# Performance work log

Hardware: AMD Instinct MI355X
Metric: run time of the kernel (lower is better)

## Reference

```python
import jax, jax.numpy as jnp
import numpy as np

EPS = 1e-7
BLOCK = 64  # block_size from init_kwargs


def project(x):
    norm = jnp.clip(jnp.linalg.norm(x, axis=-1, keepdims=True), EPS)
    return jnp.where(norm >= 1.0, x / norm * (1.0 - EPS), x)


def mobius_add(x, y, c):
    x2 = jnp.sum(x * x, -1, keepdims=True)
    y2 = jnp.sum(y * y, -1, keepdims=True)
    xy = jnp.sum(x * y, -1, keepdims=True)
    num = (1 + 2 * c * xy + c * y2) * x + (1 - c * x2) * y
    den = 1 + 2 * c * xy + c * c * x2 * y2
    return project(num / jnp.clip(den, EPS))


def logmap0(y, c):
    sqrt_c = jnp.clip(jnp.sqrt(c), EPS)
    yn = jnp.linalg.norm(y, axis=-1, keepdims=True)
    mag = jnp.arctanh(jnp.minimum(yn, 1.0 - EPS)) / sqrt_c
    return jnp.where(yn < EPS, jnp.zeros_like(y), mag * (y / jnp.clip(yn, EPS)))


def expmap0(v, c):
    sqrt_c = jnp.clip(jnp.sqrt(c), EPS)
    vn = jnp.linalg.norm(v, axis=-1, keepdims=True)
    mag = jnp.tanh(sqrt_c * jnp.clip(vn, EPS)) / sqrt_c
    return project(jnp.where(vn < EPS, jnp.zeros_like(v), mag * (v / jnp.clip(vn, EPS))))


def pdist(x, y, c):
    # x: [B,H,S,1,D], y: [B,H,1,S,D], c: [1,H,1,1,1] -> [B,H,S,S]
    sqrt_c = jnp.clip(jnp.sqrt(c), EPS)
    add_norm = jnp.linalg.norm(mobius_add(-x, y, c), axis=-1)
    sc = jnp.squeeze(sqrt_c, -1)
    arg = jnp.minimum(sc * add_norm, 1.0 - EPS)
    return 2.0 * jnp.arctanh(arg) / sc


def layernorm(x, scale, bias, eps=1e-6):
    mu = jnp.mean(x, -1, keepdims=True)
    var = jnp.mean(jnp.square(x - mu), -1, keepdims=True)
    return (x - mu) * jax.lax.rsqrt(var + eps) * scale + bias


def precompute_freqs_cis(dim, end, theta=10000.0):
    f = 1.0 / theta ** (jnp.arange(0, dim, 2, dtype=jnp.float32) / dim)
    return jnp.exp(1j * jnp.outer(jnp.arange(end), f))


def rope(x, fc):
    # split-half rotary, as in WubuBlock.apply_rotary_emb
    xr, xi = jnp.split(x, 2, -1)
    xc = jax.lax.complex(xr, xi) * fc.reshape(1, 1, fc.shape[0], fc.shape[1])
    return jnp.concatenate([xc.real, xc.imag], -1)


def setup_inputs() -> dict:
    key = jax.random.key(0)
    ks = jax.random.split(key, 8)
    B, N, D, H = 1, 1024, 512, 8
    w = lambda k, shape, s=0.02: jax.random.normal(k, shape, jnp.float32) * s
    return {
        'x': w(ks[0], (B, N, D), 0.02),  # points well inside the Poincare ball
        'c_global': jax.random.uniform(ks[1], (B, 1), jnp.float32, 0.5, 1.5),
        'W_qkv': w(ks[2], (D, 3 * D)), 'b_qkv': jnp.zeros((3 * D,), jnp.float32),
        'W_out': w(ks[3], (D, D)), 'b_out': jnp.zeros((D,), jnp.float32),
        'ln1_scale': jnp.ones((D,), jnp.float32), 'ln1_bias': jnp.zeros((D,), jnp.float32),
        'ln2_scale': jnp.ones((D,), jnp.float32), 'ln2_bias': jnp.zeros((D,), jnp.float32),
        'W_ff1': w(ks[4], (D, 4 * D)), 'b_ff1': jnp.zeros((4 * D,), jnp.float32),
        'W_ff2': w(ks[5], (4 * D, D)), 'b_ff2': jnp.zeros((D,), jnp.float32),
        'c_per_head_logits': jnp.zeros((H,), jnp.float32),
        'geo_scale': jnp.ones((1, H, 1, 1), jnp.float32),
        'start_pos': 0,
    }


def reference(x, c_global, W_qkv, b_qkv, W_out, b_out, ln1_scale, ln1_bias,
              ln2_scale, ln2_bias, W_ff1, b_ff1, W_ff2, b_ff2,
              c_per_head_logits, geo_scale, start_pos):
    B, N, D = x.shape
    H = c_per_head_logits.shape[0]
    hd = D // H
    S = BLOCK
    nb = N // S
    Be = B * nb
    xb = x.reshape(Be, S, D)
    c_b = jnp.repeat(c_global, nb, axis=0).reshape(Be, 1, 1)

    # tangent-space layernorm (norm1) then logmap to tangent for QKV proj
    xn = expmap0(layernorm(logmap0(xb, c_b), ln1_scale, ln1_bias), c_b)
    xt = logmap0(xn, c_b)
    qkv = (xt @ W_qkv + b_qkv).reshape(Be, S, 3, H, hd).transpose(2, 0, 3, 1, 4)
    q, k, v = qkv[0], qkv[1], qkv[2]  # [Be,H,S,hd]

    fc = precompute_freqs_cis(hd, S)
    q = rope(q, fc)
    k = rope(k, fc)

    c_h = jax.nn.softplus(c_per_head_logits).reshape(1, H, 1, 1)
    qh = expmap0(q, c_h)
    kh = expmap0(k, c_h)

    # full pairwise hyperbolic distance: [Be,H,S,S]
    d = pdist(qh[:, :, :, None, :], kh[:, :, None, :, :], c_h[:, :, None, :, :])
    attn = jax.nn.softmax(-geo_scale * d, axis=-1)
    ao = jnp.einsum('bhqk,bhkd->bhqd', attn, v)
    ao = ao.transpose(0, 2, 1, 3).reshape(Be, S, D)

    ah = expmap0(ao @ W_out + b_out, c_b)
    xa = mobius_add(xb, ah, c_b)  # hyperbolic residual

    # hyperbolic FFN with tangent-space norm (norm2)
    xn2 = expmap0(layernorm(logmap0(xa, c_b), ln2_scale, ln2_bias), c_b)
    t = logmap0(xn2, c_b)
    fh = expmap0(jax.nn.gelu(t @ W_ff1 + b_ff1) @ W_ff2 + b_ff2, c_b)
    out = mobius_add(xa, fh, c_b)
    return out.reshape(B, N, D)
```

## Files before the change

kernel.cpp:

```cpp
#include <hip/hip_runtime.h>
#include <math.h>

#define DEV __device__ __forceinline__
typedef _Float16 h16;
typedef __attribute__((ext_vector_type(8))) _Float16 h8v;
typedef __attribute__((ext_vector_type(4))) _Float16 h4v;
typedef __attribute__((ext_vector_type(4))) float f4v;

constexpr int NTOK = 1024;
constexpr int D    = 512;
constexpr int H    = 8;
constexpr int NB   = 16;
constexpr double EPSd = 1e-7;

DEV double wave_sum(double v) {
#pragma unroll
  for (int m = 32; m; m >>= 1) v += __shfl_xor(v, m, 64);
  return v;
}

__global__ void k_prep(const float* __restrict__ Wqkv, const float* __restrict__ Wout,
                       const float* __restrict__ Wff1, const float* __restrict__ Wff2,
                       const float* __restrict__ x, const float* __restrict__ cg,
                       const float* __restrict__ s1, const float* __restrict__ b1,
                       h16* __restrict__ qT, h16* __restrict__ oT,
                       h16* __restrict__ f1T, h16* __restrict__ f2T,
                       h16* __restrict__ xt) {
  __shared__ float t[32][33];
  const int bid = blockIdx.x;
  if (bid < 3072) {
    const float* src; h16* dh; int K, N, bx, by;
    if (bid < 768)       { src = Wqkv; dh = qT;  K = 512;  N = 1536; bx = bid % 48;          by = bid / 48; }
    else if (bid < 1024) { src = Wout; dh = oT;  K = 512;  N = 512;  bx = (bid - 768) % 16;  by = (bid - 768) / 16; }
    else if (bid < 2048) { src = Wff1; dh = f1T; K = 512;  N = 2048; bx = (bid - 1024) % 64; by = (bid - 1024) / 64; }
    else                 { src = Wff2; dh = f2T; K = 2048; N = 512;  bx = (bid - 2048) % 16; by = (bid - 2048) / 16; }
    const int n0 = bx * 32, k0 = by * 32;
    const int tx = threadIdx.x & 31, ty = threadIdx.x >> 5;
    for (int i = ty; i < 32; i += 8) t[i][tx] = src[(size_t)(k0 + i) * N + n0 + tx];
    __syncthreads();
    for (int i = ty; i < 32; i += 8)
      dh[(size_t)(n0 + i) * K + k0 + tx] = (h16)t[tx][i];
    return;
  }
  const int wid = threadIdx.x >> 6, lane = threadIdx.x & 63;
  const int tok = (bid - 3072) * 4 + wid;
  const float4* xr = (const float4*)(x + (size_t)tok * D);
  float4 xv0 = xr[lane], xv1 = xr[lane + 64];
  double sv = 0.0, svv = 0.0;
  {
    const float e[8] = {xv0.x, xv0.y, xv0.z, xv0.w, xv1.x, xv1.y, xv1.z, xv1.w};
#pragma unroll
    for (int j = 0; j < 8; ++j) { double d = e[j]; sv += d; svv += d * d; }
  }
  sv = wave_sum(sv); svv = wave_sum(svv);
  double c = (double)cg[0];
  double sc = sqrt(c); if (sc < EPSd) sc = EPSd;
  double yn = sqrt(svv);
  double arg0 = yn; if (arg0 > 1.0 - EPSd) arg0 = 1.0 - EPSd;
  double f = (yn < EPSd) ? 0.0 : atanh(arg0) / sc / fmax(yn, EPSd);
  double mu = f * sv / D;
  double var = f * f * svv / D - mu * mu;
  double rs = 1.0 / sqrt(var + 1e-6);
  const float4* s1r = (const float4*)s1;
  const float4* b1r = (const float4*)b1;
  float4 sA = s1r[lane], sB = s1r[lane + 64];
  float4 bA = b1r[lane], bB = b1r[lane + 64];
  double w[8]; double sww = 0.0;
  {
    const float e[8]  = {xv0.x, xv0.y, xv0.z, xv0.w, xv1.x, xv1.y, xv1.z, xv1.w};
    const float se[8] = {sA.x, sA.y, sA.z, sA.w, sB.x, sB.y, sB.z, sB.w};
    const float be[8] = {bA.x, bA.y, bA.z, bA.w, bB.x, bB.y, bB.z, bB.w};
#pragma unroll
    for (int j = 0; j < 8; ++j) {
      w[j] = (f * (double)e[j] - mu) * rs * (double)se[j] + (double)be[j];
      sww += w[j] * w[j];
    }
  }
  sww = wave_sum(sww);
  double vn = sqrt(sww);
  double F = 0.0;
  if (vn >= EPSd) {
    double mag_e = tanh(sc * fmax(vn, EPSd)) / sc;
    F = atanh(fmin(mag_e, 1.0 - EPSd)) / (sc * vn);
  }
  h16* dst = xt + (size_t)tok * D;
#pragma unroll
  for (int half = 0; half < 2; ++half) {
    h4v o;
#pragma unroll
    for (int e = 0; e < 4; ++e) o[e] = (h16)(float)(F * w[half * 4 + e]);
    *(h4v*)(dst + 4 * (lane + 64 * half)) = o;
  }
}

DEV void stage_tile(const h16* __restrict__ gbase, int rowstride, h16* lds,
                    int wid, int lane) {
#pragma unroll
  for (int j = 0; j < 2; ++j) {
    const int rbase = wid * 16 + j * 8;
    const int grow = rbase + (lane >> 3);
    const int gch = (lane & 7) ^ (lane >> 3);
    const h16* gp = gbase + (size_t)grow * rowstride + gch * 8;
    __builtin_amdgcn_global_load_lds(
        (const __attribute__((address_space(1))) void*)gp,
        (__attribute__((address_space(3))) void*)(lds + rbase * 64), 16, 0, 0);
  }
}
DEV h8v read_frag(const h16* lds, int row, int c) {
  const int p = c ^ (row & 7);
  return *(const h8v*)(lds + row * 64 + p * 8);
}

template <int GELU, int OHALF, int SPLITK>
__global__ __launch_bounds__(256) void k_mm(
    const h16* __restrict__ A, const h16* __restrict__ B,
    const float* __restrict__ bias, float* __restrict__ Cf, h16* __restrict__ Ch,
    int M, int N, int K) {
  __shared__ __align__(16) h16 As[2][64 * 64];
  __shared__ __align__(16) h16 Bs[2][64 * 64];
  const int tid = threadIdx.x;
  const int lane = tid & 63, wid = tid >> 6;
  const int wr = (wid >> 1) * 32, wc = (wid & 1) * 32;
  const int lr = lane & 15, lg = lane >> 4;
  const size_t r0 = (size_t)blockIdx.y * 64, c0 = (size_t)blockIdx.x * 64;
  const int kz = SPLITK ? blockIdx.z : 0;
  const int Keff = SPLITK ? (K >> 1) : K;
  const f4v z = {0.f, 0.f, 0.f, 0.f};
  f4v acc[2][2]; acc[0][0] = z; acc[0][1] = z; acc[1][0] = z; acc[1][1] = z;
  const h16* Abase = A + r0 * K + (size_t)kz * Keff;
  const h16* Bbase = B + c0 * K + (size_t)kz * Keff;
  const int NT = Keff >> 6;
  stage_tile(Abase, K, As[0], wid, lane);
  stage_tile(Bbase, K, Bs[0], wid, lane);
  __syncthreads();
  int cur = 0;
  for (int t = 0; t < NT; ++t) {
    const int nxt = cur ^ 1;
    if (t + 1 < NT) {
      stage_tile(Abase + (t + 1) * 64, K, As[nxt], wid, lane);
      stage_tile(Bbase + (t + 1) * 64, K, Bs[nxt], wid, lane);
    }
    const h16* Ac = As[cur];
    const h16* Bc = Bs[cur];
#pragma unroll
    for (int ks = 0; ks < 2; ++ks) {
      const int c = ks * 4 + lg;
      h8v a0 = read_frag(Ac, wr + lr, c);
      h8v a1 = read_frag(Ac, wr + 16 + lr, c);
      h8v b0 = read_frag(Bc, wc + lr, c);
      h8v b1 = read_frag(Bc, wc + 16 + lr, c);
      acc[0][0] = __builtin_amdgcn_mfma_f32_16x16x32_f16(a0, b0, acc[0][0], 0, 0, 0);
      acc[0][1] = __builtin_amdgcn_mfma_f32_16x16x32_f16(a0, b1, acc[0][1], 0, 0, 0);
      acc[1][0] = __builtin_amdgcn_mfma_f32_16x16x32_f16(a1, b0, acc[1][0], 0, 0, 0);
      acc[1][1] = __builtin_amdgcn_mfma_f32_16x16x32_f16(a1, b1, acc[1][1], 0, 0, 0);
    }
    __syncthreads();
    cur = nxt;
  }
  float* Cfo = Cf + (size_t)kz * M * N;
#pragma unroll
  for (int m = 0; m < 2; ++m)
#pragma unroll
    for (int n = 0; n < 2; ++n) {
      const size_t row = r0 + wr + m * 16 + lg * 4;
      const size_t col = c0 + wc + n * 16 + lr;
      const float bv = (SPLITK && kz) ? 0.f : bias[col];
#pragma unroll
      for (int e = 0; e < 4; ++e) {
        float v = acc[m][n][e] + bv;
        if (GELU) {
          float x3 = v * v * v;
          v = 0.5f * v * (1.0f + tanhf(0.7978845608028654f * (v + 0.044715f * x3)));
        }
        if (OHALF) Ch[(row + e) * N + col] = (h16)v;
        else       Cfo[(row + e) * N + col] = v;
      }
    }
}

__global__ __launch_bounds__(256) void k_attn(
    const h16* __restrict__ qkv, const float* __restrict__ chl,
    const float* __restrict__ geo, h16* __restrict__ ao) {
  __shared__ __align__(16) float Qs[64][68];
  __shared__ __align__(16) float Kt[64][68];
  __shared__ __align__(16) float Vs[64][68];
  __shared__ float q2s[64], k2s[64], fqv[64], fkv[64];
  const int be = blockIdx.x >> 3, h = blockIdx.x & 7;
  const int tid = threadIdx.x;
  const double chd = log1p(exp((double)chl[h]));
  const float ch = (float)chd;
  float sc = (float)sqrt(chd); if (sc < 1e-7f) sc = 1e-7f;
  for (int l = tid; l < 64 * 32; l += 256) {
    int s = l >> 5, j = l & 31;
    const h16* base = qkv + (size_t)(be * 64 + s) * 1536 + h * 64;
    float qa = (float)base[j],       qb = (float)base[j + 32];
    float ka = (float)base[512 + j], kb = (float)base[512 + j + 32];
    float fj = expf((float)j * -0.2878231366242557f);
    float th = (float)s * fj;
    float st, ct; sincosf(th, &st, &ct);
    Qs[s][j]      = qa * ct - qb * st;
    Qs[s][j + 32] = qa * st + qb * ct;
    Kt[j][s]      = ka * ct - kb * st;
    Kt[j + 32][s] = ka * st + kb * ct;
    Vs[s][j]      = (float)base[1024 + j];
    Vs[s][j + 32] = (float)base[1024 + j + 32];
  }
  __syncthreads();
  if (tid < 128) {
    int i = tid & 63;
    float a = 0.f;
    if (tid < 64) { for (int d2 = 0; d2 < 64; ++d2) { float v = Qs[i][d2]; a += v * v; } }
    else          { for (int d2 = 0; d2 < 64; ++d2) { float v = Kt[d2][i]; a += v * v; } }
    float n = sqrtf(a);
    float m = tanhf(sc * fmaxf(n, 1e-7f)) / sc;
    float f = (n < 1e-7f) ? 0.f : m / fmaxf(n, 1e-7f);
    if (m >= 1.f) f *= (1.f - 1e-7f) / m;
    float fn = f * n;
    if (tid < 64) { fqv[i] = f; q2s[i] = fn * fn; }
    else          { fkv[i] = f; k2s[i] = fn * fn; }
  }
  __syncthreads();
  const int i = tid >> 2, g = tid & 3;
  float gacc[16];
#pragma unroll
  for (int jj = 0; jj < 16; ++jj) gacc[jj] = 0.f;
  for (int d2 = 0; d2 < 64; ++d2) {
    float qv = Qs[i][d2];
    const float4* kp = (const float4*)&Kt[d2][g * 16];
    float4 k0 = kp[0], k1 = kp[1], k2 = kp[2], k3 = kp[3];
    gacc[0] += qv * k0.x; gacc[1] += qv * k0.y; gacc[2] += qv * k0.z; gacc[3] += qv * k0.w;
    gacc[4] += qv * k1.x; gacc[5] += qv * k1.y; gacc[6] += qv * k1.z; gacc[7] += qv * k1.w;
    gacc[8] += qv * k2.x; gacc[9] += qv * k2.y; gacc[10] += qv * k2.z; gacc[11] += qv * k2.w;
    gacc[12] += qv * k3.x; gacc[13] += qv * k3.y; gacc[14] += qv * k3.z; gacc[15] += qv * k3.w;
  }
  const float gs = geo[h];
  const float q2 = q2s[i], fqi = fqv[i];
  float lg[16];
  float mx = -1e30f;
#pragma unroll
  for (int jj = 0; jj < 16; ++jj) {
    float gq = fqi * fkv[g * 16 + jj] * gacc[jj];
    float k2 = k2s[g * 16 + jj];
    float A  = 1.f - 2.f * ch * gq + ch * k2;
    float Bv = 1.f - ch * q2;
    float n2 = fmaxf(A * A * q2 - 2.f * A * Bv * gq + Bv * Bv * k2, 0.f);
    float den = fmaxf(1.f - 2.f * ch * gq + ch * ch * q2 * k2, 1e-7f);
    float r = fminf(sqrtf(n2) / den, 1.f - 1e-7f);
    float arg = fminf(sc * r, 1.f - 1e-7f);
    float l = -gs * (2.f * atanhf(arg) / sc);
    lg[jj] = l; mx = fmaxf(mx, l);
  }
  mx = fmaxf(mx, __shfl_xor(mx, 1, 64));
  mx = fmaxf(mx, __shfl_xor(mx, 2, 64));
  float pv[16]; float sum = 0.f;
#pragma unroll
  for (int jj = 0; jj < 16; ++jj) { pv[jj] = expf(lg[jj] - mx); sum += pv[jj]; }
  sum += __shfl_xor(sum, 1, 64);
  sum += __shfl_xor(sum, 2, 64);
  float inv = 1.0f / sum;
  __syncthreads();
#pragma unroll
  for (int jj = 0; jj < 16; ++jj) Qs[i][g * 16 + jj] = pv[jj] * inv;
  __syncthreads();
  float oacc[16];
#pragma unroll
  for (int dd = 0; dd < 16; ++dd) oacc[dd] = 0.f;
  for (int jv = 0; jv < 64; ++jv) {
    float p = Qs[i][jv];
    const float4* vp = (const float4*)&Vs[jv][g * 16];
    float4 v0 = vp[0], v1 = vp[1], v2 = vp[2], v3 = vp[3];
    oacc[0] += p * v0.x; oacc[1] += p * v0.y; oacc[2] += p * v0.z; oacc[3] += p * v0.w;
    oacc[4] += p * v1.x; oacc[5] += p * v1.y; oacc[6] += p * v1.z; oacc[7] += p * v1.w;
    oacc[8] += p * v2.x; oacc[9] += p * v2.y; oacc[10] += p * v2.z; oacc[11] += p * v2.w;
    oacc[12] += p * v3.x; oacc[13] += p * v3.y; oacc[14] += p * v3.z; oacc[15] += p * v3.w;
  }
#pragma unroll
  for (int dd = 0; dd < 16; ++dd)
    ao[(size_t)(be * 64 + i) * D + h * 64 + g * 16 + dd] = (h16)oacc[dd];
}

__global__ void k_resid(const float* __restrict__ x, const float* __restrict__ proj,
                        const float* __restrict__ cg, const float* __restrict__ s2,
                        const float* __restrict__ b2, float* __restrict__ xa,
                        h16* __restrict__ t2) {
  const int wid = threadIdx.x >> 6, lane = threadIdx.x & 63;
  const int tok = blockIdx.x * 4 + wid;
  const float4* xr  = (const float4*)(x + (size_t)tok * D);
  const float4* p0r = (const float4*)(proj + (size_t)tok * D);
  const float4* p1r = (const float4*)(proj + (size_t)NTOK * D + (size_t)tok * D);
  float4 xv0 = xr[lane], xv1 = xr[lane + 64];
  float4 pa0 = p0r[lane], pa1 = p0r[lane + 64];
  float4 pb0 = p1r[lane], pb1 = p1r[lane + 64];
  float pe[8], xe[8];
  xe[0]=xv0.x; xe[1]=xv0.y; xe[2]=xv0.z; xe[3]=xv0.w; xe[4]=xv1.x; xe[5]=xv1.y; xe[6]=xv1.z; xe[7]=xv1.w;
  pe[0]=pa0.x+pb0.x; pe[1]=pa0.y+pb0.y; pe[2]=pa0.z+pb0.z; pe[3]=pa0.w+pb0.w;
  pe[4]=pa1.x+pb1.x; pe[5]=pa1.y+pb1.y; pe[6]=pa1.z+pb1.z; pe[7]=pa1.w+pb1.w;
  double sx = 0, sp = 0, xx = 0, pp = 0, xp = 0;
#pragma unroll
  for (int j = 0; j < 8; ++j) {
    double dx = xe[j], dp = pe[j];
    sx += dx; sp += dp; xx += dx * dx; pp += dp * dp; xp += dx * dp;
  }
  sx = wave_sum(sx); sp = wave_sum(sp); xx = wave_sum(xx);
  pp = wave_sum(pp); xp = wave_sum(xp);
  double c = (double)cg[0];
  double sc = sqrt(c); if (sc < EPSd) sc = EPSd;
  double pn = sqrt(pp);
  double me = tanh(sc * fmax(pn, EPSd)) / sc;
  double fs = (pn < EPSd) ? 0.0 : me / fmax(pn, EPSd);
  if (me >= 1.0) fs *= (1.0 - EPSd) / me;
  double y2 = fs * fs * pp, xy = fs * xp;
  double a = 1.0 + 2.0 * c * xy + c * y2;
  double b = 1.0 - c * xx;
  double den = 1.0 + 2.0 * c * xy + c * c * xx * y2;
  if (den < EPSd) den = EPSd;
  double zn = sqrt(fmax(a * a * xx + 2.0 * a * b * xy + b * b * y2, 0.0)) / den;
  double zs = 1.0 / den;
  if (zn >= 1.0) zs *= (1.0 - EPSd) / zn;
  double xan = (zn >= 1.0) ? (1.0 - EPSd) : zn;
  double A0 = zs * a, B0 = zs * b * fs;
  double xav[8];
#pragma unroll
  for (int j = 0; j < 8; ++j) xav[j] = A0 * (double)xe[j] + B0 * (double)pe[j];
  {
    float4 o0 = {(float)xav[0], (float)xav[1], (float)xav[2], (float)xav[3]};
    float4 o1 = {(float)xav[4], (float)xav[5], (float)xav[6], (float)xav[7]};
    float4* xw = (float4*)(xa + (size_t)tok * D);
    xw[lane] = o0; xw[lane + 64] = o1;
  }
  double sxa  = A0 * sx + B0 * sp;
  double sxa2 = A0 * A0 * xx + 2.0 * A0 * B0 * xp + B0 * B0 * pp;
  double fl = 0.0;
  if (xan >= EPSd) fl = atanh(fmin(xan, 1.0 - EPSd)) / (sc * fmax(xan, EPSd));
  double mu = fl * sxa / D;
  double var = fl * fl * sxa2 / D - mu * mu;
  double rs = 1.0 / sqrt(var + 1e-6);
  const float4* s2r = (const float4*)s2;
  const float4* b2r = (const float4*)b2;
  float4 sA = s2r[lane], sB = s2r[lane + 64];
  float4 bA = b2r[lane], bB = b2r[lane + 64];
  const float se[8] = {sA.x, sA.y, sA.z, sA.w, sB.x, sB.y, sB.z, sB.w};
  const float be[8] = {bA.x, bA.y, bA.z, bA.w, bB.x, bB.y, bB.z, bB.w};
  double w[8]; double sww = 0.0;
#pragma unroll
  for (int j = 0; j < 8; ++j) {
    w[j] = (fl * xav[j] - mu) * rs * (double)se[j] + (double)be[j];
    sww += w[j] * w[j];
  }
  sww = wave_sum(sww);
  double vn = sqrt(sww);
  double F = 0.0;
  if (vn >= EPSd) {
    double mag_e = tanh(sc * fmax(vn, EPSd)) / sc;
    F = atanh(fmin(mag_e, 1.0 - EPSd)) / (sc * vn);
  }
  h16* dst = t2 + (size_t)tok * D;
#pragma unroll
  for (int half = 0; half < 2; ++half) {
    h4v o;
#pragma unroll
    for (int e = 0; e < 4; ++e) o[e] = (h16)(float)(F * w[half * 4 + e]);
    *(h4v*)(dst + 4 * (lane + 64 * half)) = o;
  }
}

__global__ void k_final(const float* __restrict__ xa, const float* __restrict__ f2,
                        const float* __restrict__ cg, float* __restrict__ out) {
  const int wid = threadIdx.x >> 6, lane = threadIdx.x & 63;
  const int tok = blockIdx.x * 4 + wid;
  const float4* ar  = (const float4*)(xa + (size_t)tok * D);
  const float4* f0r = (const float4*)(f2 + (size_t)tok * D);
  const float4* f1r = (const float4*)(f2 + (size_t)NTOK * D + (size_t)tok * D);
  float4 xv0 = ar[lane], xv1 = ar[lane + 64];
  float4 pa0 = f0r[lane], pa1 = f0r[lane + 64];
  float4 pb0 = f1r[lane], pb1 = f1r[lane + 64];
  float pe[8], xe[8];
  xe[0]=xv0.x; xe[1]=xv0.y; xe[2]=xv0.z; xe[3]=xv0.w; xe[4]=xv1.x; xe[5]=xv1.y; xe[6]=xv1.z; xe[7]=xv1.w;
  pe[0]=pa0.x+pb0.x; pe[1]=pa0.y+pb0.y; pe[2]=pa0.z+pb0.z; pe[3]=pa0.w+pb0.w;
  pe[4]=pa1.x+pb1.x; pe[5]=pa1.y+pb1.y; pe[6]=pa1.z+pb1.z; pe[7]=pa1.w+pb1.w;
  double xx = 0, pp = 0, xp = 0;
#pragma unroll
  for (int j = 0; j < 8; ++j) {
    double dx = xe[j], dp = pe[j];
    xx += dx * dx; pp += dp * dp; xp += dx * dp;
  }
  xx = wave_sum(xx); pp = wave_sum(pp); xp = wave_sum(xp);
  double c = (double)cg[0];
  double sc = sqrt(c); if (sc < EPSd) sc = EPSd;
  double pn = sqrt(pp);
  double me = tanh(sc * fmax(pn, EPSd)) / sc;
  double fs = (pn < EPSd) ? 0.0 : me / fmax(pn, EPSd);
  if (me >= 1.0) fs *= (1.0 - EPSd) / me;
  double y2 = fs * fs * pp, xy = fs * xp;
  double a = 1.0 + 2.0 * c * xy + c * y2;
  double b = 1.0 - c * xx;
  double den = 1.0 + 2.0 * c * xy + c * c * xx * y2;
  if (den < EPSd) den = EPSd;
  double zn = sqrt(fmax(a * a * xx + 2.0 * a * b * xy + b * b * y2, 0.0)) / den;
  double zs = 1.0 / den;
  if (zn >= 1.0) zs *= (1.0 - EPSd) / zn;
  double A0 = zs * a, B0 = zs * b * fs;
  float4 o0, o1;
  o0.x = (float)(A0 * xe[0] + B0 * pe[0]); o0.y = (float)(A0 * xe[1] + B0 * pe[1]);
  o0.z = (float)(A0 * xe[2] + B0 * pe[2]); o0.w = (float)(A0 * xe[3] + B0 * pe[3]);
  o1.x = (float)(A0 * xe[4] + B0 * pe[4]); o1.y = (float)(A0 * xe[5] + B0 * pe[5]);
  o1.z = (float)(A0 * xe[6] + B0 * pe[6]); o1.w = (float)(A0 * xe[7] + B0 * pe[7]);
  float4* ow = (float4*)(out + (size_t)tok * D);
  ow[lane] = o0; ow[lane + 64] = o1;
}

extern "C" void kernel_launch(void* const* d_in, const int* in_sizes, int n_in,
                              void* d_out, int out_size, void* d_ws, size_t ws_size,
                              hipStream_t stream) {
  (void)in_sizes; (void)n_in; (void)out_size; (void)ws_size;
  const float* x    = (const float*)d_in[0];
  const float* cg   = (const float*)d_in[1];
  const float* Wqkv = (const float*)d_in[2];
  const float* bqkv = (const float*)d_in[3];
  const float* Wout = (const float*)d_in[4];
  const float* bout = (const float*)d_in[5];
  const float* s1   = (const float*)d_in[6];
  const float* b1   = (const float*)d_in[7];
  const float* s2   = (const float*)d_in[8];
  const float* b2   = (const float*)d_in[9];
  const float* Wff1 = (const float*)d_in[10];
  const float* bff1 = (const float*)d_in[11];
  const float* Wff2 = (const float*)d_in[12];
  const float* bff2 = (const float*)d_in[13];
  const float* chl  = (const float*)d_in[14];
  const float* geo  = (const float*)d_in[15];
  float* out = (float*)d_out;

  char* base = (char*)d_ws;
  const size_t MB = 1024 * 1024;
  h16*   WqkvT = (h16*)(base + 0);
  h16*   WoutT = (h16*)(base + (3*MB)/2);
  h16*   Wff1T = (h16*)(base + 2*MB);
  h16*   Wff2T = (h16*)(base + 4*MB);
  h16*   xt    = (h16*)(base + 6*MB);
  h16*   qkv   = (h16*)(base + 7*MB);
  h16*   ao    = (h16*)(base + 10*MB);
  float* proj  = (float*)(base + 11*MB);
  float* xa    = (float*)(base + 7*MB);
  h16*   t2    = (h16*)(base + 6*MB);
  h16*   h1    = (h16*)(base + 11*MB);
  float* f2    = (float*)(base + 0);

  k_prep<<<3072 + NTOK / 4, 256, 0, stream>>>(Wqkv, Wout, Wff1, Wff2, x, cg, s1, b1,
                                              WqkvT, WoutT, Wff1T, Wff2T, xt);
  k_mm<0, 1, 0><<<dim3(1536 / 64, NTOK / 64), 256, 0, stream>>>(
      xt, WqkvT, bqkv, nullptr, qkv, NTOK, 1536, 512);
  k_attn<<<NB * H, 256, 0, stream>>>(qkv, chl, geo, ao);
  k_mm<0, 0, 1><<<dim3(512 / 64, NTOK / 64, 2), 256, 0, stream>>>(
      ao, WoutT, bout, proj, nullptr, NTOK, 512, 512);
  k_resid<<<NTOK / 4, 256, 0, stream>>>(x, proj, cg, s2, b2, xa, t2);
  k_mm<1, 1, 0><<<dim3(2048 / 64, NTOK / 64), 256, 0, stream>>>(
      t2, Wff1T, bff1, nullptr, h1, NTOK, 2048, 512);
  k_mm<0, 0, 1><<<dim3(512 / 64, NTOK / 64, 2), 256, 0, stream>>>(
      h1, Wff2T, bff2, f2, nullptr, NTOK, 512, 2048);
  k_final<<<NTOK / 4, 256, 0, stream>>>(xa, f2, cg, out);
}
```

Measured before the change: 78.01 us.

## Split attention queries across two blocks and relax GEMM pipeline barriers

```diff
diff --git a/kernel.cpp b/kernel.cpp
--- a/kernel.cpp
+++ b/kernel.cpp
@@ -132,14 +132,17 @@
   const int NT = Keff >> 6;
   stage_tile(Abase, K, As[0], wid, lane);
   stage_tile(Bbase, K, Bs[0], wid, lane);
-  __syncthreads();
   int cur = 0;
   for (int t = 0; t < NT; ++t) {
     const int nxt = cur ^ 1;
     if (t + 1 < NT) {
       stage_tile(Abase + (t + 1) * 64, K, As[nxt], wid, lane);
       stage_tile(Bbase + (t + 1) * 64, K, Bs[nxt], wid, lane);
+      asm volatile("s_waitcnt vmcnt(4)" ::: "memory");
+    } else {
+      asm volatile("s_waitcnt vmcnt(0)" ::: "memory");
     }
+    asm volatile("s_barrier" ::: "memory");
     const h16* Ac = As[cur];
     const h16* Bc = Bs[cur];
 #pragma unroll
@@ -154,7 +157,7 @@
       acc[1][0] = __builtin_amdgcn_mfma_f32_16x16x32_f16(a1, b0, acc[1][0], 0, 0, 0);
       acc[1][1] = __builtin_amdgcn_mfma_f32_16x16x32_f16(a1, b1, acc[1][1], 0, 0, 0);
     }
-    __syncthreads();
+    asm volatile("s_barrier" ::: "memory");
     cur = nxt;
   }
   float* Cfo = Cf + (size_t)kz * M * N;
@@ -181,11 +184,12 @@
 __global__ __launch_bounds__(256) void k_attn(
     const h16* __restrict__ qkv, const float* __restrict__ chl,
     const float* __restrict__ geo, h16* __restrict__ ao) {
-  __shared__ __align__(16) float Qs[64][68];
+  __shared__ __align__(16) float Qs[32][68];
   __shared__ __align__(16) float Kt[64][68];
   __shared__ __align__(16) float Vs[64][68];
-  __shared__ float q2s[64], k2s[64], fqv[64], fkv[64];
-  const int be = blockIdx.x >> 3, h = blockIdx.x & 7;
+  __shared__ float q2s[32], k2s[64], fqv[32], fkv[64];
+  const int bid = blockIdx.x;
+  const int be = bid >> 4, h = (bid >> 1) & 7, q0 = (bid & 1) * 32;
   const int tid = threadIdx.x;
   const double chd = log1p(exp((double)chl[h]));
   const float ch = (float)chd;
@@ -193,54 +197,64 @@
   for (int l = tid; l < 64 * 32; l += 256) {
     int s = l >> 5, j = l & 31;
     const h16* base = qkv + (size_t)(be * 64 + s) * 1536 + h * 64;
-    float qa = (float)base[j],       qb = (float)base[j + 32];
     float ka = (float)base[512 + j], kb = (float)base[512 + j + 32];
     float fj = expf((float)j * -0.2878231366242557f);
-    float th = (float)s * fj;
-    float st, ct; sincosf(th, &st, &ct);
-    Qs[s][j]      = qa * ct - qb * st;
-    Qs[s][j + 32] = qa * st + qb * ct;
+    float st, ct; sincosf((float)s * fj, &st, &ct);
     Kt[j][s]      = ka * ct - kb * st;
     Kt[j + 32][s] = ka * st + kb * ct;
     Vs[s][j]      = (float)base[1024 + j];
     Vs[s][j + 32] = (float)base[1024 + j + 32];
   }
+  for (int l = tid; l < 32 * 32; l += 256) {
+    int s = l >> 5, j = l & 31;
+    const h16* base = qkv + (size_t)(be * 64 + q0 + s) * 1536 + h * 64;
+    float qa = (float)base[j], qb = (float)base[j + 32];
+    float fj = expf((float)j * -0.2878231366242557f);
+    float st, ct; sincosf((float)(q0 + s) * fj, &st, &ct);
+    Qs[s][j]      = qa * ct - qb * st;
+    Qs[s][j + 32] = qa * st + qb * ct;
+  }
   __syncthreads();
-  if (tid < 128) {
-    int i = tid & 63;
+  if (tid < 64) {
     float a = 0.f;
-    if (tid < 64) { for (int d2 = 0; d2 < 64; ++d2) { float v = Qs[i][d2]; a += v * v; } }
-    else          { for (int d2 = 0; d2 < 64; ++d2) { float v = Kt[d2][i]; a += v * v; } }
+    for (int d2 = 0; d2 < 64; ++d2) { float v = Kt[d2][tid]; a += v * v; }
     float n = sqrtf(a);
     float m = tanhf(sc * fmaxf(n, 1e-7f)) / sc;
     float f = (n < 1e-7f) ? 0.f : m / fmaxf(n, 1e-7f);
     if (m >= 1.f) f *= (1.f - 1e-7f) / m;
     float fn = f * n;
-    if (tid < 64) { fqv[i] = f; q2s[i] = fn * fn; }
-    else          { fkv[i] = f; k2s[i] = fn * fn; }
+    fkv[tid] = f; k2s[tid] = fn * fn;
+  } else if (tid < 96) {
+    int i = tid - 64;
+    float a = 0.f;
+    for (int d2 = 0; d2 < 64; ++d2) { float v = Qs[i][d2]; a += v * v; }
+    float n = sqrtf(a);
+    float m = tanhf(sc * fmaxf(n, 1e-7f)) / sc;
+    float f = (n < 1e-7f) ? 0.f : m / fmaxf(n, 1e-7f);
+    if (m >= 1.f) f *= (1.f - 1e-7f) / m;
+    float fn = f * n;
+    fqv[i] = f; q2s[i] = fn * fn;
   }
   __syncthreads();
-  const int i = tid >> 2, g = tid & 3;
-  float gacc[16];
-#pragma unroll
-  for (int jj = 0; jj < 16; ++jj) gacc[jj] = 0.f;
+  const int i = tid >> 3, g = tid & 7;
+  float gacc[8];
+#pragma unroll
+  for (int jj = 0; jj < 8; ++jj) gacc[jj] = 0.f;
   for (int d2 = 0; d2 < 64; ++d2) {
     float qv = Qs[i][d2];
-    const float4* kp = (const float4*)&Kt[d2][g * 16];
-    float4 k0 = kp[0], k1 = kp[1], k2 = kp[2], k3 = kp[3];
+    const float4* kp = (const float4*)&Kt[d2][g * 8];
+    float4 k0 = kp[0], k1 = kp[1];
     gacc[0] += qv * k0.x; gacc[1] += qv * k0.y; gacc[2] += qv * k0.z; gacc[3] += qv * k0.w;
     gacc[4] += qv * k1.x; gacc[5] += qv * k1.y; gacc[6] += qv * k1.z; gacc[7] += qv * k1.w;
-    gacc[8] += qv * k2.x; gacc[9] += qv * k2.y; gacc[10] += qv * k2.z; gacc[11] += qv * k2.w;
-    gacc[12] += qv * k3.x; gacc[13] += qv * k3.y; gacc[14] += qv * k3.z; gacc[15] += qv * k3.w;
   }
   const float gs = geo[h];
   const float q2 = q2s[i], fqi = fqv[i];
-  float lg[16];
+  float lg[8];
   float mx = -1e30f;
 #pragma unroll
-  for (int jj = 0; jj < 16; ++jj) {
-    float gq = fqi * fkv[g * 16 + jj] * gacc[jj];
-    float k2 = k2s[g * 16 + jj];
+  for (int jj = 0; jj < 8; ++jj) {
+    float gq = fqi * fkv[g * 8 + jj] * gacc[jj];
+    float k2 = k2s[g * 8 + jj];
     float A  = 1.f - 2.f * ch * gq + ch * k2;
     float Bv = 1.f - ch * q2;
     float n2 = fmaxf(A * A * q2 - 2.f * A * Bv * gq + Bv * Bv * k2, 0.f);
@@ -252,31 +266,29 @@
   }
   mx = fmaxf(mx, __shfl_xor(mx, 1, 64));
   mx = fmaxf(mx, __shfl_xor(mx, 2, 64));
-  float pv[16]; float sum = 0.f;
-#pragma unroll
-  for (int jj = 0; jj < 16; ++jj) { pv[jj] = expf(lg[jj] - mx); sum += pv[jj]; }
+  mx = fmaxf(mx, __shfl_xor(mx, 4, 64));
+  float pv[8]; float sum = 0.f;
+#pragma unroll
+  for (int jj = 0; jj < 8; ++jj) { pv[jj] = expf(lg[jj] - mx); sum += pv[jj]; }
   sum += __shfl_xor(sum, 1, 64);
   sum += __shfl_xor(sum, 2, 64);
+  sum += __shfl_xor(sum, 4, 64);
   float inv = 1.0f / sum;
-  __syncthreads();
-#pragma unroll
-  for (int jj = 0; jj < 16; ++jj) Qs[i][g * 16 + jj] = pv[jj] * inv;
-  __syncthreads();
-  float oacc[16];
-#pragma unroll
-  for (int dd = 0; dd < 16; ++dd) oacc[dd] = 0.f;
+#pragma unroll
+  for (int jj = 0; jj < 8; ++jj) Qs[i][g * 8 + jj] = pv[jj] * inv;
+  float oacc[8];
+#pragma unroll
+  for (int dd = 0; dd < 8; ++dd) oacc[dd] = 0.f;
   for (int jv = 0; jv < 64; ++jv) {
     float p = Qs[i][jv];
-    const float4* vp = (const float4*)&Vs[jv][g * 16];
-    float4 v0 = vp[0], v1 = vp[1], v2 = vp[2], v3 = vp[3];
+    const float4* vp = (const float4*)&Vs[jv][g * 8];
+    float4 v0 = vp[0], v1 = vp[1];
     oacc[0] += p * v0.x; oacc[1] += p * v0.y; oacc[2] += p * v0.z; oacc[3] += p * v0.w;
     oacc[4] += p * v1.x; oacc[5] += p * v1.y; oacc[6] += p * v1.z; oacc[7] += p * v1.w;
-    oacc[8] += p * v2.x; oacc[9] += p * v2.y; oacc[10] += p * v2.z; oacc[11] += p * v2.w;
-    oacc[12] += p * v3.x; oacc[13] += p * v3.y; oacc[14] += p * v3.z; oacc[15] += p * v3.w;
-  }
-#pragma unroll
-  for (int dd = 0; dd < 16; ++dd)
-    ao[(size_t)(be * 64 + i) * D + h * 64 + g * 16 + dd] = (h16)oacc[dd];
+  }
+#pragma unroll
+  for (int dd = 0; dd < 8; ++dd)
+    ao[(size_t)(be * 64 + q0 + i) * D + h * 64 + g * 8 + dd] = (h16)oacc[dd];
 }
 
 __global__ void k_resid(const float* __restrict__ x, const float* __restrict__ proj,
@@ -450,7 +462,7 @@
                                               WqkvT, WoutT, Wff1T, Wff2T, xt);
   k_mm<0, 1, 0><<<dim3(1536 / 64, NTOK / 64), 256, 0, stream>>>(
       xt, WqkvT, bqkv, nullptr, qkv, NTOK, 1536, 512);
-  k_attn<<<NB * H, 256, 0, stream>>>(qkv, chl, geo, ao);
+  k_attn<<<NB * H * 2, 256, 0, stream>>>(qkv, chl, geo, ao);
   k_mm<0, 0, 1><<<dim3(512 / 64, NTOK / 64, 2), 256, 0, stream>>>(
       ao, WoutT, bout, proj, nullptr, NTOK, 512, 512);
   k_resid<<<NTOK / 4, 256, 0, stream>>>(x, proj, cg, s2, b2, xa, t2);
```

After: 74.89 us. 1.04x faster.
